# Optimization experiments

Hardware: AMD Instinct MI355X
Metric: run time of the kernel (lower is better)

## Reference

```python
import jax, jax.numpy as jnp
import numpy as np
import math

B, L, IN_DIM, OUT_DIM = 2, 2048, 128, 128
H, DH = 8, 32            # num_heads, dim_head
ED = H * DH * 2          # embed_dim = 512
DEPTH = 1
LAMBDA_INIT = 0.8 - 0.6 * math.exp(-0.3 * (DEPTH + 1))
EPS = 1e-8


def setup_inputs() -> dict:
    key = jax.random.key(0)
    ks = jax.random.split(key, 10)
    x = jax.random.normal(ks[0], (B, 1, L, IN_DIM), dtype=jnp.float32)
    mask_2d = jax.random.bernoulli(ks[1], 0.9, (B, L, L))
    Wq = jax.random.normal(ks[2], (IN_DIM, ED), dtype=jnp.float32) * 0.05
    Wkv = jax.random.normal(ks[3], (IN_DIM, 2 * ED), dtype=jnp.float32) * 0.05
    Wout = jax.random.normal(ks[4], (ED, OUT_DIM), dtype=jnp.float32) * 0.05
    lambda_q1 = jax.random.normal(ks[5], (DH,), dtype=jnp.float32) * 0.1
    lambda_k1 = jax.random.normal(ks[6], (DH,), dtype=jnp.float32) * 0.1
    lambda_q2 = jax.random.normal(ks[7], (DH,), dtype=jnp.float32) * 0.1
    lambda_k2 = jax.random.normal(ks[8], (DH,), dtype=jnp.float32) * 0.1
    gamma = jnp.ones((2 * DH,), dtype=jnp.float32)
    return {"x": x, "mask_2d": mask_2d, "Wq": Wq, "Wkv": Wkv, "Wout": Wout,
            "lambda_q1": lambda_q1, "lambda_k1": lambda_k1,
            "lambda_q2": lambda_q2, "lambda_k2": lambda_k2, "gamma": gamma}


def reference(x, mask_2d, Wq, Wkv, Wout, lambda_q1, lambda_k1, lambda_q2, lambda_k2, gamma):
    b = x.shape[0]
    xs = x[:, 0]                                   # [b, L, in_dim]
    q = xs @ Wq                                    # [b, L, 2*H*DH]
    k, v = jnp.split(xs @ Wkv, 2, axis=-1)
    q = q.reshape(b, L, 2 * H, DH).transpose(0, 2, 1, 3) * (DH ** -0.5)  # [b,2H,L,d]
    k = k.reshape(b, L, 2 * H, DH).transpose(0, 2, 1, 3)                 # [b,2H,L,d]
    v = v.reshape(b, L, H, 2 * DH).transpose(0, 2, 1, 3)                 # [b,H,L,2d]
    dots = jnp.einsum('bnld,bnmd->bnlm', q, k)     # [b,2H,L,L]
    mask_value = -jnp.finfo(dots.dtype).max
    dots = jnp.where(mask_2d[:, None, :, :], dots, mask_value)
    attn_w = jax.nn.softmax(dots.astype(jnp.float32), axis=-1).astype(dots.dtype)
    lam1 = jnp.exp(jnp.sum(lambda_q1 * lambda_k1))
    lam2 = jnp.exp(jnp.sum(lambda_q2 * lambda_k2))
    lam = lam1 - lam2 + LAMBDA_INIT
    attn_w = attn_w.reshape(b, H, 2, L, L)
    attn_w = attn_w[:, :, 0] - lam * attn_w[:, :, 1]   # [b,H,L,L]
    attn = jnp.einsum('bhlm,bhmd->bhld', attn_w, v)    # [b,H,L,2d]
    rms = jnp.sqrt(jnp.mean(attn ** 2, axis=-1, keepdims=True))
    attn = gamma * (attn / (rms + EPS)) * (1.0 - LAMBDA_INIT)
    out = attn.transpose(0, 2, 1, 3).reshape(b, L, H * 2 * DH) @ Wout  # [b,L,out_dim]
    return out[:, None]                             # [b,1,L,out_dim]
```

## Files before the change

kernel.cpp:

```cpp
#include <hip/hip_runtime.h>
#include <float.h>
#include <math.h>

typedef __attribute__((ext_vector_type(8))) short short8;
typedef __attribute__((ext_vector_type(4))) float f32x4;
typedef __attribute__((ext_vector_type(4))) unsigned short ushort4v;

constexpr int SEQL = 2048;
constexpr int NQH  = 16;
constexpr int NVH  = 8;
constexpr int DHD  = 32;
constexpr float LAMB_INIT = 0.4707130183436648f;
constexpr float REPS      = 1e-8f;
constexpr float QW        = 0.25503492f;

static __device__ __forceinline__ unsigned short f2bf(float f) {
    union { float f; unsigned u; } a; a.f = f;
    unsigned u = a.u;
    u += 0x7fffu + ((u >> 16) & 1u);
    return (unsigned short)(u >> 16);
}

static __device__ __forceinline__ float bf2f(unsigned short s) {
    union { unsigned u; float f; } a; a.u = ((unsigned)s) << 16;
    return a.f;
}

static __device__ __forceinline__ unsigned cvtpk(float lo, float hi) {
    unsigned r;
    asm("v_cvt_pk_bf16_f32 %0, %1, %2" : "=v"(r) : "v"(lo), "v"(hi));
    return r;
}

static __device__ __forceinline__ float expv(float x) {
    float r;
    asm("v_exp_f32 %0, %1" : "=v"(r) : "v"(x));
    return r;
}

static __device__ __forceinline__ void stage16(const unsigned short* g, unsigned short* l) {
    __builtin_amdgcn_global_load_lds(
        (const __attribute__((address_space(1))) unsigned int*)g,
        (__attribute__((address_space(3))) unsigned int*)l, 16, 0, 0);
}

__global__ __launch_bounds__(256) void pack_prep_kernel(
        const unsigned char* __restrict__ mb, const int* __restrict__ mi,
        unsigned long long* __restrict__ bits,
        const float* __restrict__ x, const float* __restrict__ Wq,
        const float* __restrict__ Wkv, const float* __restrict__ Wout,
        unsigned short* __restrict__ xb, unsigned short* __restrict__ Wf,
        unsigned short* __restrict__ WfO) {
    __shared__ int cnt[256];
    int t = threadIdx.x;
    int c = 0;
    #pragma unroll
    for (int i = 0; i < 16; ++i) c += (mb[t * 16 + i] != 0);
    cnt[t] = c;
    __syncthreads();
    for (int s = 128; s > 0; s >>= 1) { if (t < s) cnt[t] += cnt[t + s]; __syncthreads(); }
    int f = cnt[0] > 2048;
    int gtid = blockIdx.x * 256 + t;
    int nthr = gridDim.x * 256;
    {
        const int total = 2 * SEQL * (SEQL / 64);
        int wid = blockIdx.x * 4 + (t >> 6);
        int lane = t & 63;
        int stride = gridDim.x * 4;
        for (int w = wid; w < total; w += stride) {
            int e = w * 64 + lane;
            int v = f ? (int)mb[e] : mi[e];
            unsigned long long b = __ballot(v != 0);
            if (lane == 0) bits[w] = b;
        }
    }
    {
        float4 v = ((const float4*)x)[gtid];
        ushort4v o = { f2bf(v.x), f2bf(v.y), f2bf(v.z), f2bf(v.w) };
        ((ushort4v*)xb)[gtid] = o;
    }
    for (int e = gtid; e < 262144; e += nthr) {
        int k = e >> 11, cc = e & 2047;
        if (cc < 1536) {
            float v = (cc < 512) ? Wq[(size_t)k * 512 + cc] * QW
                                 : Wkv[(size_t)k * 1024 + (cc - 512)];
            int cp = cc >> 4, lr = cc & 15, kk = k >> 5, lg = (k >> 3) & 3, j = k & 7;
            Wf[(((size_t)(cp * 4 + kk) * 4 + lg) * 16 + lr) * 8 + j] = f2bf(v);
        }
    }
    if (gtid < 65536) {
        int k = gtid >> 7, cc = gtid & 127;
        float v = Wout[gtid];
        int cp = cc >> 4, lr = cc & 15, kk = k >> 5, lg = (k >> 3) & 3, j = k & 7;
        WfO[(((size_t)(cp * 16 + kk) * 4 + lg) * 16 + lr) * 8 + j] = f2bf(v);
    }
}

__global__ __launch_bounds__(256) void qkv_mfma_kernel(
        const unsigned short* __restrict__ xb, const unsigned short* __restrict__ Wf,
        unsigned short* __restrict__ Q, unsigned short* __restrict__ Kf,
        unsigned short* __restrict__ Vf) {
    int t = threadIdx.x, w = t >> 6, lane = t & 63, lr = lane & 15, lg = lane >> 4;
    int lid = blockIdx.x;
    int swz = (lid & 7) * 192 + (lid >> 3);
    int by = swz >> 6, bx = swz & 63;
    int r0 = bx * 64 + w * 16;
    short8 ax[4];
    #pragma unroll
    for (int kk = 0; kk < 4; ++kk)
        ax[kk] = *(const short8*)(xb + (size_t)(r0 + lr) * 128 + kk * 32 + lg * 8);
    f32x4 acc[4];
    #pragma unroll
    for (int ct = 0; ct < 4; ++ct) acc[ct] = (f32x4){0.f, 0.f, 0.f, 0.f};
    #pragma unroll
    for (int ct = 0; ct < 4; ++ct) {
        int cp = by * 4 + ct;
        #pragma unroll
        for (int kk = 0; kk < 4; ++kk) {
            short8 bw = *(const short8*)(Wf + (size_t)(cp * 4 + kk) * 512 + lane * 8);
            acc[ct] = __builtin_amdgcn_mfma_f32_16x16x32_bf16(ax[kk], bw, acc[ct], 0, 0, 0);
        }
    }
    int gr0 = r0 + 4 * lg;
    int b = gr0 >> 11;
    if (by < 8) {
        #pragma unroll
        for (int ct = 0; ct < 4; ++ct) {
            int col = by * 64 + 16 * ct + lr;
            int n = col >> 5, d = col & 31;
            #pragma unroll
            for (int r = 0; r < 4; ++r) {
                int l = (gr0 + r) & 2047;
                Q[(((size_t)(b * NQH + n)) * SEQL + l) * DHD + d] = f2bf(acc[ct][r]);
            }
        }
    } else if (by < 16) {
        #pragma unroll
        for (int ct = 0; ct < 4; ++ct) {
            int ck = by * 64 + 16 * ct + lr - 512;
            int n = ck >> 5, dk = ck & 31;
            size_t hb = ((size_t)(b * NQH + n)) * 65536 + (dk >> 3) * 128 + (dk & 7);
            #pragma unroll
            for (int r = 0; r < 4; ++r) {
                int l = (gr0 + r) & 2047;
                Kf[hb + (size_t)((l >> 6) * 4 + ((l >> 4) & 3)) * 512 + (l & 15) * 8]
                    = f2bf(acc[ct][r]);
            }
        }
    } else {
        #pragma unroll
        for (int ct = 0; ct < 4; ++ct) {
            int cv = by * 64 + 16 * ct + lr - 1024;
            int h = cv >> 6, d = cv & 63;
            size_t hb = ((size_t)(b * NVH + h)) * 131072 + (d >> 4) * 512 + (d & 15) * 8;
            #pragma unroll
            for (int r = 0; r < 4; ++r) {
                int l = (gr0 + r) & 2047;
                Vf[hb + (size_t)((l >> 6) * 2 + ((l >> 5) & 1)) * 2048
                      + ((l >> 4) & 1) * 4 + ((l >> 2) & 3) * 128 + (l & 3)]
                    = f2bf(acc[ct][r]);
            }
        }
    }
}

__global__ __launch_bounds__(256, 4) void attn_kernel(
        const unsigned short* __restrict__ Q, const unsigned short* __restrict__ Kf,
        const unsigned short* __restrict__ Vf, const unsigned long long* __restrict__ bits,
        unsigned short* __restrict__ O) {
    __shared__ unsigned short lds[3][6144];
    int tid = threadIdx.x;
    int w = tid >> 6, lane = tid & 63;
    int lr = lane & 15, lg = lane >> 4;
    int lid = blockIdx.y * 32 + blockIdx.x;
    int swz = (lid & 7) * 128 + (lid >> 3);
    int qtile = swz & 31, bn = swz >> 5;
    int b = bn >> 4, n = bn & 15, vh = n >> 1;
    int q0 = qtile * 64 + w * 16;

    short8 aq = *(const short8*)(Q + (((size_t)bn) * SEQL + q0 + lr) * DHD + lg * 8);
    const unsigned short* KH = Kf + ((size_t)bn) * 65536;
    const unsigned short* VH = Vf + ((size_t)(b * NVH + vh)) * 131072;
    const unsigned long long* mrow = bits + ((size_t)b * SEQL + q0 + lr) * 32;

    auto stage_tile = [&](int bf, int it) {
        #pragma unroll
        for (int j = 0; j < 3; ++j) {
            int c = 3 * w + j;
            const unsigned short* src = (c < 4)
                ? (KH + (size_t)it * 2048 + c * 512)
                : (VH + (size_t)it * 4096 + (c - 4) * 512);
            stage16(src + lane * 8, &lds[bf][c * 512]);
        }
    };

    f32x4 oacc[4];
    #pragma unroll
    for (int m = 0; m < 4; ++m) oacc[m] = (f32x4){0.f, 0.f, 0.f, 0.f};
    float ssum = 0.f;
    const f32x4 Z = {0.f, 0.f, 0.f, 0.f};

    stage_tile(0, 0);
    stage_tile(1, 1);
    unsigned long long mw = mrow[0];

    for (int t = 0; t < 32; ++t) {
        asm volatile("s_waitcnt vmcnt(4)" ::: "memory");
        __builtin_amdgcn_s_barrier();
        __builtin_amdgcn_sched_barrier(0);
        stage_tile((t + 2) % 3, (t + 2) & 31);
        unsigned long long mwc = mw;
        mw = mrow[(t + 1) & 31];
        __builtin_amdgcn_sched_barrier(0);
        const unsigned short* L = &lds[t % 3][0];
        short8 bk[4], bv[8];
        #pragma unroll
        for (int c = 0; c < 4; ++c) bk[c] = *(const short8*)(L + c * 512 + lane * 8);
        #pragma unroll
        for (int z = 0; z < 8; ++z) bv[z] = *(const short8*)(L + 2048 + z * 512 + lane * 8);
        f32x4 s[4];
        __builtin_amdgcn_s_setprio(1);
        #pragma unroll
        for (int c = 0; c < 4; ++c)
            s[c] = __builtin_amdgcn_mfma_f32_16x16x32_bf16(bk[c], aq, Z, 0, 0, 0);
        __builtin_amdgcn_s_setprio(0);
        unsigned long long mwl = mwc >> (4 * lg);
        unsigned mlo = (unsigned)mwl, mhi = (unsigned)(mwl >> 32);
        float p[4][4];
        #pragma unroll
        for (int c = 0; c < 4; ++c) {
            unsigned wv = (c < 2) ? mlo : mhi;
            int sh = (c & 1) * 16;
            #pragma unroll
            for (int r = 0; r < 4; ++r) {
                unsigned keep = (wv >> (sh + r)) & 1u;
                float e = expv(s[c][r]);
                p[c][r] = keep ? e : 0.f;
            }
        }
        float ac = 0.f;
        #pragma unroll
        for (int c = 0; c < 4; ++c)
            #pragma unroll
            for (int r = 0; r < 4; ++r) ac += p[c][r];
        ssum += ac;
        union { short8 v; unsigned u[4]; } a0, a1;
        a0.u[0] = cvtpk(p[0][0], p[0][1]); a0.u[1] = cvtpk(p[0][2], p[0][3]);
        a0.u[2] = cvtpk(p[1][0], p[1][1]); a0.u[3] = cvtpk(p[1][2], p[1][3]);
        a1.u[0] = cvtpk(p[2][0], p[2][1]); a1.u[1] = cvtpk(p[2][2], p[2][3]);
        a1.u[2] = cvtpk(p[3][0], p[3][1]); a1.u[3] = cvtpk(p[3][2], p[3][3]);
        __builtin_amdgcn_s_setprio(1);
        #pragma unroll
        for (int m = 0; m < 4; ++m)
            oacc[m] = __builtin_amdgcn_mfma_f32_16x16x32_bf16(a0.v, bv[m], oacc[m], 0, 0, 0);
        #pragma unroll
        for (int m = 0; m < 4; ++m)
            oacc[m] = __builtin_amdgcn_mfma_f32_16x16x32_bf16(a1.v, bv[4 + m], oacc[m], 0, 0, 0);
        __builtin_amdgcn_s_setprio(0);
    }
    asm volatile("s_waitcnt vmcnt(0)" ::: "memory");
    ssum += __shfl_xor(ssum, 16, 64);
    ssum += __shfl_xor(ssum, 32, 64);
    float inv = 1.f / ssum;
    float invr[4];
    #pragma unroll
    for (int r = 0; r < 4; ++r) invr[r] = __shfl(inv, 4 * lg + r, 64);
    unsigned short* Ob = O + (((size_t)bn) * SEQL + q0 + 4 * lg) * 64 + lr;
    #pragma unroll
    for (int m = 0; m < 4; ++m)
        #pragma unroll
        for (int r = 0; r < 4; ++r)
            Ob[(size_t)r * 64 + 16 * m] = f2bf(oacc[m][r] * invr[r]);
}

__global__ __launch_bounds__(256) void merge_kernel(
        const unsigned short* __restrict__ O,
        const float* __restrict__ lq1, const float* __restrict__ lk1,
        const float* __restrict__ lq2, const float* __restrict__ lk2,
        const float* __restrict__ gamma, unsigned short* __restrict__ Ab) {
    int t = threadIdx.x;
    int T = blockIdx.x * 256 + t;
    int row = T >> 2, part = T & 3;
    int b = row >> 14, h = (row >> 11) & 7, l = row & 2047;
    int l31 = t & 31;
    float t1 = lq1[l31] * lk1[l31];
    float t2 = lq2[l31] * lk2[l31];
    #pragma unroll
    for (int o = 1; o < 32; o <<= 1) { t1 += __shfl_xor(t1, o, 64); t2 += __shfl_xor(t2, o, 64); }
    float lam = __expf(t1) - __expf(t2) + LAMB_INIT;
    const unsigned short* p1 = O + (((size_t)(b * NQH + 2 * h)) * SEQL + l) * 64 + part * 16;
    const unsigned short* p2 = p1 + (size_t)SEQL * 64;
    short8 a0 = *(const short8*)p1, a1 = *(const short8*)(p1 + 8);
    short8 b0 = *(const short8*)p2, b1 = *(const short8*)(p2 + 8);
    float v[16]; float sq = 0.f;
    #pragma unroll
    for (int i = 0; i < 8; ++i) {
        v[i]     = bf2f((unsigned short)a0[i]) - lam * bf2f((unsigned short)b0[i]);
        v[8 + i] = bf2f((unsigned short)a1[i]) - lam * bf2f((unsigned short)b1[i]);
    }
    #pragma unroll
    for (int i = 0; i < 16; ++i) sq += v[i] * v[i];
    sq += __shfl_xor(sq, 1, 64);
    sq += __shfl_xor(sq, 2, 64);
    float sc = (1.f - LAMB_INIT) / (sqrtf(sq * (1.f / 64.f)) + REPS);
    unsigned short* dst = Ab + ((size_t)(b * SEQL + l)) * 512 + h * 64 + part * 16;
    short8 o0, o1;
    #pragma unroll
    for (int i = 0; i < 8; ++i) {
        o0[i] = (short)f2bf(v[i]     * sc * gamma[part * 16 + i]);
        o1[i] = (short)f2bf(v[8 + i] * sc * gamma[part * 16 + 8 + i]);
    }
    *(short8*)dst = o0;
    *(short8*)(dst + 8) = o1;
}

__global__ __launch_bounds__(64) void proj_mfma_kernel(
        const unsigned short* __restrict__ Ab, const unsigned short* __restrict__ WfO,
        float* __restrict__ out) {
    int lane = threadIdx.x & 63, lr = lane & 15, lg = lane >> 4;
    int r0 = blockIdx.x * 16;
    f32x4 acc[8];
    #pragma unroll
    for (int ct = 0; ct < 8; ++ct) acc[ct] = (f32x4){0.f, 0.f, 0.f, 0.f};
    #pragma unroll
    for (int kk = 0; kk < 16; ++kk) {
        short8 af = *(const short8*)(Ab + (size_t)(r0 + lr) * 512 + kk * 32 + lg * 8);
        #pragma unroll
        for (int ct = 0; ct < 8; ++ct) {
            short8 bf = *(const short8*)(WfO + (size_t)(ct * 16 + kk) * 512 + lane * 8);
            acc[ct] = __builtin_amdgcn_mfma_f32_16x16x32_bf16(af, bf, acc[ct], 0, 0, 0);
        }
    }
    #pragma unroll
    for (int ct = 0; ct < 8; ++ct)
        #pragma unroll
        for (int r = 0; r < 4; ++r)
            out[(size_t)(r0 + 4 * lg + r) * 128 + ct * 16 + lr] = acc[ct][r];
}

extern "C" void kernel_launch(void* const* d_in, const int* in_sizes, int n_in,
                              void* d_out, int out_size, void* d_ws, size_t ws_size,
                              hipStream_t stream) {
    const float* x    = (const float*)d_in[0];
    const void*  mask = d_in[1];
    const float* Wq   = (const float*)d_in[2];
    const float* Wkv  = (const float*)d_in[3];
    const float* Wout = (const float*)d_in[4];
    const float* lq1  = (const float*)d_in[5];
    const float* lk1  = (const float*)d_in[6];
    const float* lq2  = (const float*)d_in[7];
    const float* lk2  = (const float*)d_in[8];
    const float* gam  = (const float*)d_in[9];
    float* out = (float*)d_out;

    char* wsb = (char*)d_ws;
    unsigned long long* bits = (unsigned long long*)(wsb + 4096);
    unsigned short* Q        = (unsigned short*)(wsb + 1052672);
    unsigned short* Kf       = (unsigned short*)(wsb + 5246976);
    unsigned short* Vf       = (unsigned short*)(wsb + 9441280);
    unsigned short* xb       = (unsigned short*)(wsb + 13635584);
    unsigned short* Wf       = (unsigned short*)(wsb + 14684160);
    unsigned short* WfO      = (unsigned short*)(wsb + 15077376);
    unsigned short* Ab       = (unsigned short*)(wsb + 15208448);
    unsigned short* O        = (unsigned short*)(wsb + 19402752);

    pack_prep_kernel<<<512, 256, 0, stream>>>((const unsigned char*)mask,
                                              (const int*)mask, bits,
                                              x, Wq, Wkv, Wout, xb, Wf, WfO);
    qkv_mfma_kernel<<<1536, 256, 0, stream>>>(xb, Wf, Q, Kf, Vf);
    attn_kernel<<<dim3(32, 32), 256, 0, stream>>>(Q, Kf, Vf, bits, O);
    merge_kernel<<<512, 256, 0, stream>>>(O, lq1, lk1, lq2, lk2, gam, Ab);
    proj_mfma_kernel<<<256, 64, 0, stream>>>(Ab, WfO, out);
}
```

Before: 100.2 us.

## Fuse differential merge and RMS norm into attention kernel, pairing heads per block

The attention kernel now runs 512 threads per block that handle both query heads of a differential pair. They share one V tile staged in LDS and exchange normalized outputs through LDS to apply the lambda subtraction, RMS norm and gamma scaling in-kernel. This removes the separate merge kernel and the bf16 round trip of the intermediate O tensor through global memory. It also halves the V staging traffic per pair. In exchange, half the waves sit idle during the epilogue, block count halves, and LDS use per block grows, which could lower occupancy.

```diff
diff --git a/kernel.cpp b/kernel.cpp
--- a/kernel.cpp
+++ b/kernel.cpp
@@ -19,11 +19,6 @@
     unsigned u = a.u;
     u += 0x7fffu + ((u >> 16) & 1u);
     return (unsigned short)(u >> 16);
-}
-
-static __device__ __forceinline__ float bf2f(unsigned short s) {
-    union { unsigned u; float f; } a; a.u = ((unsigned)s) << 16;
-    return a.f;
 }
 
 static __device__ __forceinline__ unsigned cvtpk(float lo, float hi) {
@@ -164,32 +159,38 @@
     }
 }
 
-__global__ __launch_bounds__(256, 4) void attn_kernel(
+__global__ __launch_bounds__(512, 2) void attn_kernel(
         const unsigned short* __restrict__ Q, const unsigned short* __restrict__ Kf,
         const unsigned short* __restrict__ Vf, const unsigned long long* __restrict__ bits,
-        unsigned short* __restrict__ O) {
-    __shared__ unsigned short lds[3][6144];
+        const float* __restrict__ lq1, const float* __restrict__ lk1,
+        const float* __restrict__ lq2, const float* __restrict__ lk2,
+        const float* __restrict__ gamma, unsigned short* __restrict__ Ab) {
+    __shared__ unsigned short lds[3][8192];
     int tid = threadIdx.x;
     int w = tid >> 6, lane = tid & 63;
     int lr = lane & 15, lg = lane >> 4;
+    int ws = w & 3, hh = w >> 2;
     int lid = blockIdx.y * 32 + blockIdx.x;
-    int swz = (lid & 7) * 128 + (lid >> 3);
-    int qtile = swz & 31, bn = swz >> 5;
-    int b = bn >> 4, n = bn & 15, vh = n >> 1;
-    int q0 = qtile * 64 + w * 16;
+    int swz = (lid & 7) * 64 + (lid >> 3);
+    int qtile = swz & 31, bp = swz >> 5;
+    int b = bp >> 3, h = bp & 7;
+    int q0 = qtile * 64 + ws * 16;
+    int bnA = b * NQH + 2 * h;
+    int bn = bnA + hh;
 
     short8 aq = *(const short8*)(Q + (((size_t)bn) * SEQL + q0 + lr) * DHD + lg * 8);
-    const unsigned short* KH = Kf + ((size_t)bn) * 65536;
-    const unsigned short* VH = Vf + ((size_t)(b * NVH + vh)) * 131072;
+    const unsigned short* KH2 = Kf + ((size_t)bnA) * 65536;
+    const unsigned short* VH  = Vf + ((size_t)(b * NVH + h)) * 131072;
     const unsigned long long* mrow = bits + ((size_t)b * SEQL + q0 + lr) * 32;
 
     auto stage_tile = [&](int bf, int it) {
         #pragma unroll
-        for (int j = 0; j < 3; ++j) {
-            int c = 3 * w + j;
-            const unsigned short* src = (c < 4)
-                ? (KH + (size_t)it * 2048 + c * 512)
-                : (VH + (size_t)it * 4096 + (c - 4) * 512);
+        for (int j = 0; j < 2; ++j) {
+            int c = 2 * w + j;
+            const unsigned short* src =
+                (c < 4) ? (KH2 + (size_t)it * 2048 + c * 512)
+              : (c < 8) ? (KH2 + 65536 + (size_t)it * 2048 + (c - 4) * 512)
+                        : (VH + (size_t)it * 4096 + (c - 8) * 512);
             stage16(src + lane * 8, &lds[bf][c * 512]);
         }
     };
@@ -205,7 +206,7 @@
     unsigned long long mw = mrow[0];
 
     for (int t = 0; t < 32; ++t) {
-        asm volatile("s_waitcnt vmcnt(4)" ::: "memory");
+        asm volatile("s_waitcnt vmcnt(3)" ::: "memory");
         __builtin_amdgcn_s_barrier();
         __builtin_amdgcn_sched_barrier(0);
         stage_tile((t + 2) % 3, (t + 2) & 31);
@@ -215,9 +216,11 @@
         const unsigned short* L = &lds[t % 3][0];
         short8 bk[4], bv[8];
         #pragma unroll
-        for (int c = 0; c < 4; ++c) bk[c] = *(const short8*)(L + c * 512 + lane * 8);
-        #pragma unroll
-        for (int z = 0; z < 8; ++z) bv[z] = *(const short8*)(L + 2048 + z * 512 + lane * 8);
+        for (int c = 0; c < 4; ++c)
+            bk[c] = *(const short8*)(L + hh * 2048 + c * 512 + lane * 8);
+        #pragma unroll
+        for (int z = 0; z < 8; ++z)
+            bv[z] = *(const short8*)(L + 4096 + z * 512 + lane * 8);
         f32x4 s[4];
         __builtin_amdgcn_s_setprio(1);
         #pragma unroll
@@ -259,59 +262,59 @@
         __builtin_amdgcn_s_setprio(0);
     }
     asm volatile("s_waitcnt vmcnt(0)" ::: "memory");
+    __syncthreads();
     ssum += __shfl_xor(ssum, 16, 64);
     ssum += __shfl_xor(ssum, 32, 64);
     float inv = 1.f / ssum;
     float invr[4];
     #pragma unroll
     for (int r = 0; r < 4; ++r) invr[r] = __shfl(inv, 4 * lg + r, 64);
-    unsigned short* Ob = O + (((size_t)bn) * SEQL + q0 + 4 * lg) * 64 + lr;
+    float on[4][4];
     #pragma unroll
     for (int m = 0; m < 4; ++m)
         #pragma unroll
-        for (int r = 0; r < 4; ++r)
-            Ob[(size_t)r * 64 + 16 * m] = f2bf(oacc[m][r] * invr[r]);
-}
-
-__global__ __launch_bounds__(256) void merge_kernel(
-        const unsigned short* __restrict__ O,
-        const float* __restrict__ lq1, const float* __restrict__ lk1,
-        const float* __restrict__ lq2, const float* __restrict__ lk2,
-        const float* __restrict__ gamma, unsigned short* __restrict__ Ab) {
-    int t = threadIdx.x;
-    int T = blockIdx.x * 256 + t;
-    int row = T >> 2, part = T & 3;
-    int b = row >> 14, h = (row >> 11) & 7, l = row & 2047;
-    int l31 = t & 31;
+        for (int r = 0; r < 4; ++r) on[m][r] = oacc[m][r] * invr[r];
+    float* fb = (float*)&lds[0][0];
+    if (hh) {
+        #pragma unroll
+        for (int m = 0; m < 4; ++m)
+            #pragma unroll
+            for (int r = 0; r < 4; ++r)
+                fb[ws * 1088 + lane * 17 + m * 4 + r] = on[m][r];
+    }
+    __syncthreads();
+    if (hh) return;
+    int l31 = lane & 31;
     float t1 = lq1[l31] * lk1[l31];
     float t2 = lq2[l31] * lk2[l31];
     #pragma unroll
     for (int o = 1; o < 32; o <<= 1) { t1 += __shfl_xor(t1, o, 64); t2 += __shfl_xor(t2, o, 64); }
     float lam = __expf(t1) - __expf(t2) + LAMB_INIT;
-    const unsigned short* p1 = O + (((size_t)(b * NQH + 2 * h)) * SEQL + l) * 64 + part * 16;
-    const unsigned short* p2 = p1 + (size_t)SEQL * 64;
-    short8 a0 = *(const short8*)p1, a1 = *(const short8*)(p1 + 8);
-    short8 b0 = *(const short8*)p2, b1 = *(const short8*)(p2 + 8);
-    float v[16]; float sq = 0.f;
-    #pragma unroll
-    for (int i = 0; i < 8; ++i) {
-        v[i]     = bf2f((unsigned short)a0[i]) - lam * bf2f((unsigned short)b0[i]);
-        v[8 + i] = bf2f((unsigned short)a1[i]) - lam * bf2f((unsigned short)b1[i]);
-    }
-    #pragma unroll
-    for (int i = 0; i < 16; ++i) sq += v[i] * v[i];
-    sq += __shfl_xor(sq, 1, 64);
-    sq += __shfl_xor(sq, 2, 64);
-    float sc = (1.f - LAMB_INIT) / (sqrtf(sq * (1.f / 64.f)) + REPS);
-    unsigned short* dst = Ab + ((size_t)(b * SEQL + l)) * 512 + h * 64 + part * 16;
-    short8 o0, o1;
-    #pragma unroll
-    for (int i = 0; i < 8; ++i) {
-        o0[i] = (short)f2bf(v[i]     * sc * gamma[part * 16 + i]);
-        o1[i] = (short)f2bf(v[8 + i] * sc * gamma[part * 16 + 8 + i]);
-    }
-    *(short8*)dst = o0;
-    *(short8*)(dst + 8) = o1;
+    float dv[4][4];
+    float sq[4] = {0.f, 0.f, 0.f, 0.f};
+    #pragma unroll
+    for (int m = 0; m < 4; ++m)
+        #pragma unroll
+        for (int r = 0; r < 4; ++r) {
+            float v = on[m][r] - lam * fb[ws * 1088 + lane * 17 + m * 4 + r];
+            dv[m][r] = v;
+            sq[r] += v * v;
+        }
+    #pragma unroll
+    for (int r = 0; r < 4; ++r) {
+        #pragma unroll
+        for (int o = 1; o < 16; o <<= 1) sq[r] += __shfl_xor(sq[r], o, 64);
+        sq[r] = (1.f - LAMB_INIT) / (sqrtf(sq[r] * (1.f / 64.f)) + REPS);
+    }
+    float gm[4];
+    #pragma unroll
+    for (int m = 0; m < 4; ++m) gm[m] = gamma[16 * m + lr];
+    unsigned short* Abp = Ab + ((size_t)(b * SEQL + q0 + 4 * lg)) * 512 + h * 64 + lr;
+    #pragma unroll
+    for (int m = 0; m < 4; ++m)
+        #pragma unroll
+        for (int r = 0; r < 4; ++r)
+            Abp[(size_t)r * 512 + 16 * m] = f2bf(dv[m][r] * sq[r] * gm[m]);
 }
 
 __global__ __launch_bounds__(64) void proj_mfma_kernel(
@@ -362,13 +365,12 @@
     unsigned short* Wf       = (unsigned short*)(wsb + 14684160);
     unsigned short* WfO      = (unsigned short*)(wsb + 15077376);
     unsigned short* Ab       = (unsigned short*)(wsb + 15208448);
-    unsigned short* O        = (unsigned short*)(wsb + 19402752);
 
     pack_prep_kernel<<<512, 256, 0, stream>>>((const unsigned char*)mask,
                                               (const int*)mask, bits,
                                               x, Wq, Wkv, Wout, xb, Wf, WfO);
     qkv_mfma_kernel<<<1536, 256, 0, stream>>>(xb, Wf, Q, Kf, Vf);
-    attn_kernel<<<dim3(32, 32), 256, 0, stream>>>(Q, Kf, Vf, bits, O);
-    merge_kernel<<<512, 256, 0, stream>>>(O, lq1, lk1, lq2, lk2, gam, Ab);
+    attn_kernel<<<dim3(32, 16), 512, 0, stream>>>(Q, Kf, Vf, bits,
+                                                  lq1, lk1, lq2, lk2, gam, Ab);
     proj_mfma_kernel<<<256, 64, 0, stream>>>(Ab, WfO, out);
 }
```

Result: faster. 96.72 us (-3.5%).
